# Kernel optimization log

Measured on AMD Instinct MI355X. Metric: run time of the kernel, lower is better.

The kernel has to match this reference:

```python
import jax, jax.numpy as jnp
import numpy as np

T = 1048576          # number of time steps in the trace
SIGMA_NUM = 8
EPSILON_NUM = 8
FEAT = 2 + SIGMA_NUM + EPSILON_NUM  # [t, r_obs, sigmas..., epsilons...]


def setup_inputs() -> dict:
    key = jax.random.key(0)
    ks = jax.random.split(key, 6)
    trace = jax.random.normal(ks[0], (T, FEAT), dtype=jnp.float32)
    # column 0 is time: sorted grid with small dt so the 1M-step recurrence stays bounded
    trace = trace.at[:, 0].set(jnp.arange(T, dtype=jnp.float32) * 1e-3)
    # column 1 row 0 is the initial rate; keep it positive-ish
    trace = trace.at[0, 1].set(0.05)
    sigma_W = jax.random.normal(ks[1], (1, SIGMA_NUM), dtype=jnp.float32) * 0.01
    sigma_b = jax.random.normal(ks[2], (1,), dtype=jnp.float32) * 0.01
    eps_W = jax.random.normal(ks[3], (1, EPSILON_NUM), dtype=jnp.float32) * 0.01
    k = jnp.abs(jax.random.normal(ks[4], (1,), dtype=jnp.float32)) * 0.1
    theta = jnp.abs(jax.random.normal(ks[5], (1,), dtype=jnp.float32)) * 0.05
    return {"trace_data": trace, "sigma_W": sigma_W, "sigma_b": sigma_b,
            "eps_W": eps_W, "k": k, "theta": theta}


def reference(trace_data, sigma_W, sigma_b, eps_W, k, theta):
    S, E = SIGMA_NUM, EPSILON_NUM
    t = trace_data[:, 0]
    dts = t[1:] - t[:-1]                                   # [T-1]
    # sigma/epsilon projections depend only on trace data -> vectorize outside scan
    sig = trace_data[:-1, 2:2 + S] @ sigma_W[0] + sigma_b[0]   # [T-1]
    eps = trace_data[:-1, 2 + S:2 + S + E] @ eps_W[0]          # [T-1]
    kk = k[0]
    th = theta[0]
    r0 = trace_data[0, 1]

    def step(r, x):
        dt, s, e = x
        ode = r + kk * (th - r) * dt
        sde = s * jnp.sqrt(jnp.abs(r * dt)) * e
        r_next = ode + sde
        return r_next, r_next

    _, r_predicts = jax.lax.scan(step, r0, (dts, sig, eps))   # [T-1]
    regs = 2.0 * kk * th - sig ** 2                           # [T-1]
    return r_predicts, regs, dts
```

## Files before the change

kernel.cpp:

```cpp
#include <hip/hip_runtime.h>
#include <math.h>

#define NSTEPS   1048575
#define FEAT     18
#define NB1      1024
#define NT1      256
#define NQ       (NB1 * NT1)
#define SLOTS    608
#define WBYTES   (SLOTS * 16)

#define GLDS16(g, l) \
    __builtin_amdgcn_global_load_lds((const __attribute__((address_space(1))) void*)(g), \
                                     (__attribute__((address_space(3))) void*)(l), 16, 0, 0)

#define WAIT_VM0()   asm volatile("s_waitcnt vmcnt(0)" ::: "memory")
#define WAIT_LGKM0() asm volatile("s_waitcnt lgkmcnt(0)" ::: "memory")

#define GSTEP(dd, cc) { \
    float a   = fmaf(-k, (dd), 1.f); \
    float b   = kth * (dd); \
    float ar  = fabsf(r); \
    float sq  = sqrtf(ar); \
    float inv = (ar > 1e-30f) ? rsqrtf(ar) : 0.f; \
    float g   = fmaf(0.5f * (cc), copysignf(inv, r), a); \
    r = fmaf((cc), sq, fmaf(a, r, b)); \
    P *= g; }

#define FSTEP(dd, cc) { \
    float a = fmaf(-k, (dd), 1.f); \
    float b = kth * (dd); \
    rr = fmaf((cc), sqrtf(fabsf(rr)), fmaf(a, rr, b)); }

#define DOTSE(S0,S1,S2,S3,S4,S5,S6,S7, E0,E1,E2,E3,E4,E5,E6,E7, sigv, epv) { \
    float sig_ = sb0; \
    sig_ = fmaf((S0), sw0, sig_); sig_ = fmaf((S1), sw1, sig_); \
    sig_ = fmaf((S2), sw2, sig_); sig_ = fmaf((S3), sw3, sig_); \
    sig_ = fmaf((S4), sw4, sig_); sig_ = fmaf((S5), sw5, sig_); \
    sig_ = fmaf((S6), sw6, sig_); sig_ = fmaf((S7), sw7, sig_); \
    float ep_ = 0.f; \
    ep_ = fmaf((E0), ew0, ep_); ep_ = fmaf((E1), ew1, ep_); \
    ep_ = fmaf((E2), ew2, ep_); ep_ = fmaf((E3), ew3, ep_); \
    ep_ = fmaf((E4), ew4, ep_); ep_ = fmaf((E5), ew5, ep_); \
    ep_ = fmaf((E6), ew6, ep_); ep_ = fmaf((E7), ew7, ep_); \
    (sigv) = sig_; (epv) = ep_; }

#define EXTRACT_COMPUTE(JROW) { \
    const float4* sr = (const float4*)lw + 19 * (JROW); \
    float4 u0 = sr[0],  u1  = sr[1],  u2  = sr[2],  u3  = sr[3],  u4  = sr[4]; \
    float4 u5 = sr[5],  u6  = sr[6],  u7  = sr[7],  u8  = sr[8]; \
    float4 u9 = sr[9],  u10 = sr[10], u11 = sr[11], u12 = sr[12], u13 = sr[13]; \
    float4 u14 = sr[14], u15 = sr[15], u16 = sr[16], u17 = sr[17]; \
    tfirst = u0.x; t3 = u13.z; \
    d0 = u4.z  - u0.x;  d1 = u9.x - u4.z;  d2 = u13.z - u9.x; \
    float ep0, ep1, ep2; \
    DOTSE(u0.z,u0.w,u1.x,u1.y,u1.z,u1.w,u2.x,u2.y, \
          u2.z,u2.w,u3.x,u3.y,u3.z,u3.w,u4.x,u4.y, sig0, ep0) \
    DOTSE(u5.x,u5.y,u5.z,u5.w,u6.x,u6.y,u6.z,u6.w, \
          u7.x,u7.y,u7.z,u7.w,u8.x,u8.y,u8.z,u8.w, sig1, ep1) \
    DOTSE(u9.z,u9.w,u10.x,u10.y,u10.z,u10.w,u11.x,u11.y, \
          u11.z,u11.w,u12.x,u12.y,u12.z,u12.w,u13.x,u13.y, sig2, ep2) \
    DOTSE(u14.x,u14.y,u14.z,u14.w,u15.x,u15.y,u15.z,u15.w, \
          u16.x,u16.y,u16.z,u16.w,u17.x,u17.y,u17.z,u17.w, sig3, ep3) \
    c0v = sig0 * ep0 * sqrtf(fabsf(d0)); \
    c1v = sig1 * ep1 * sqrtf(fabsf(d1)); \
    c2v = sig2 * ep2 * sqrtf(fabsf(d2)); }

__device__ __forceinline__ void stage_pass(const float4* __restrict__ base4,
                                           char* lds_wave, int lane)
{
    int jr = lane / 19;
    int ic = lane - 19 * jr;
#pragma unroll
    for (int i = 0; i < 10; ++i) {
        int col = (ic == 18) ? 17 : ic;
        const float4* src = base4 + (18 * jr + col);
        if (i < 9) {
            GLDS16(src, lds_wave + i * 1024);
        } else if (lane < 32) {
            GLDS16(src, lds_wave + 9 * 1024);
        }
        jr += 3; ic += 7;
        if (ic >= 19) { ic -= 19; ++jr; }
    }
}

__device__ __forceinline__ void wave_scan_affine(float& A, float& B, int lane) {
#pragma unroll
    for (int d = 1; d < 64; d <<= 1) {
        float pA = __shfl_up(A, d, 64);
        float pB = __shfl_up(B, d, 64);
        if (lane >= d) { B = fmaf(A, pB, B); A *= pA; }
    }
}

__global__ void __launch_bounds__(NT1) cir_prep(
    const float* __restrict__ trace,
    const float* __restrict__ sW, const float* __restrict__ sb,
    const float* __restrict__ eW, const float* __restrict__ kp,
    const float* __restrict__ thp,
    float* __restrict__ out,
    float2* __restrict__ dc, float2* __restrict__ pref, float2* __restrict__ agg)
{
    __shared__ __align__(16) char stage[4 * WBYTES];
    __shared__ float wAs[4], wBs[4];

    const int tid = threadIdx.x, lane = tid & 63, wid = tid >> 6, bid = blockIdx.x;
    const long c = (long)bid * NT1 + tid;
    char* lw = stage + wid * WBYTES;
    const float4* t4 = (const float4*)trace;
    const long waveQuad = (long)bid * NT1 + (long)wid * 64;

    stage_pass(t4 + waveQuad * 18, lw, lane);

    const float k = kp[0], th = thp[0], kth = k * th, tkth2 = 2.f * kth;
    const float sb0 = sb[0];
    const float sw0 = sW[0], sw1 = sW[1], sw2 = sW[2], sw3 = sW[3];
    const float sw4 = sW[4], sw5 = sW[5], sw6 = sW[6], sw7 = sW[7];
    const float ew0 = eW[0], ew1 = eW[1], ew2 = eW[2], ew3 = eW[3];
    const float ew4 = eW[4], ew5 = eW[5], ew6 = eW[6], ew7 = eW[7];
    const float t0g = trace[0], r0v = trace[1];

    float tfirst, t3, d0, d1, d2, c0v, c1v, c2v, sig0, sig1, sig2, sig3, ep3;

    WAIT_VM0();
    if (lane < 32) EXTRACT_COMPUTE(lane)
    WAIT_LGKM0();

    stage_pass(t4 + (waveQuad + 32) * 18, lw, lane);
    WAIT_VM0();
    if (lane >= 32) EXTRACT_COMPUTE(lane - 32)

    float tnext = __shfl_down(tfirst, 1, 64);
    if (lane == 63)
        tnext = (c + 1 < (long)NQ) ? trace[(c * 4 + 4) * FEAT] : 0.f;
    float d3 = tnext - t3;
    const long n0 = c * 4;
    float c3v = sig3 * ep3 * sqrtf(fabsf(d3));
    if (n0 + 4 > NSTEPS) { d3 = 0.f; c3v = 0.f; }

    out[NSTEPS + n0 + 0] = fmaf(-sig0, sig0, tkth2);
    out[NSTEPS + n0 + 1] = fmaf(-sig1, sig1, tkth2);
    out[NSTEPS + n0 + 2] = fmaf(-sig2, sig2, tkth2);
    out[2L * NSTEPS + n0 + 0] = d0;
    out[2L * NSTEPS + n0 + 1] = d1;
    out[2L * NSTEPS + n0 + 2] = d2;
    if (n0 + 4 <= NSTEPS) {
        out[NSTEPS + n0 + 3] = fmaf(-sig3, sig3, tkth2);
        out[2L * NSTEPS + n0 + 3] = d3;
    }

    float4* dc4 = (float4*)dc;
    dc4[2 * c]     = make_float4(d0, c0v, d1, c1v);
    dc4[2 * c + 1] = make_float4(d2, c2v, d3, c3v);

    float s = th + (r0v - th) * __expf(-k * (tfirst - t0g));
    float r = s, P = 1.f;
    GSTEP(d0, c0v)
    GSTEP(d1, c1v)
    GSTEP(d2, c2v)
    GSTEP(d3, c3v)
    float A = P, Bv = fmaf(-P, s, r);

    float iA = A, iB = Bv;
    wave_scan_affine(iA, iB, lane);
    if (lane == 63) { wAs[wid] = iA; wBs[wid] = iB; }
    __syncthreads();
    if (wid == 0) {
        float aA = (lane < 4) ? wAs[lane] : 1.f;
        float aB = (lane < 4) ? wBs[lane] : 0.f;
        wave_scan_affine(aA, aB, lane);
        if (lane < 4) { wAs[lane] = aA; wBs[lane] = aB; }
    }
    __syncthreads();
    float weA = 1.f, weB = 0.f;
    if (wid > 0) { weA = wAs[wid - 1]; weB = wBs[wid - 1]; }
    float eA = __shfl_up(iA, 1, 64), eB = __shfl_up(iB, 1, 64);
    if (lane == 0) { eA = 1.f; eB = 0.f; }

    pref[c] = make_float2(eA * weA, fmaf(eA, weB, eB));
    if (tid == 0) agg[bid] = make_float2(wAs[3], wBs[3]);
}

__global__ void __launch_bounds__(NT1) cir_final(
    const float* __restrict__ trace,
    const float* __restrict__ kp, const float* __restrict__ thp,
    const float2* __restrict__ dc, const float2* __restrict__ pref,
    const float2* __restrict__ agg,
    float* __restrict__ out)
{
    __shared__ float2 incs[NB1];
    __shared__ float wA2[4], wB2[4];

    const int tid = threadIdx.x, lane = tid & 63, wid = tid >> 6, bid = blockIdx.x;
    const long c = (long)bid * NT1 + tid;
    const float k = kp[0], th = thp[0], kth = k * th;
    const float r0v = trace[1];

    float2 a0 = agg[4 * tid + 0], a1 = agg[4 * tid + 1];
    float2 a2 = agg[4 * tid + 2], a3 = agg[4 * tid + 3];
    float cA = a0.x, cB = a0.y;
    cB = fmaf(a1.x, cB, a1.y); cA *= a1.x;
    cB = fmaf(a2.x, cB, a2.y); cA *= a2.x;
    cB = fmaf(a3.x, cB, a3.y); cA *= a3.x;

    float iA = cA, iB = cB;
    wave_scan_affine(iA, iB, lane);
    if (lane == 63) { wA2[wid] = iA; wB2[wid] = iB; }
    __syncthreads();
    if (wid == 0) {
        float aA = (lane < 4) ? wA2[lane] : 1.f;
        float aB = (lane < 4) ? wB2[lane] : 0.f;
        wave_scan_affine(aA, aB, lane);
        if (lane < 4) { wA2[lane] = aA; wB2[lane] = aB; }
    }
    __syncthreads();
    float weA = 1.f, weB = 0.f;
    if (wid > 0) { weA = wA2[wid - 1]; weB = wB2[wid - 1]; }
    float eA = __shfl_up(iA, 1, 64), eB = __shfl_up(iB, 1, 64);
    if (lane == 0) { eA = 1.f; eB = 0.f; }
    float EA = eA * weA, EB = fmaf(eA, weB, eB);

    float xA = a0.x * EA,  xB = fmaf(a0.x, EB, a0.y);
    incs[4 * tid + 0] = make_float2(xA, xB);
    xB = fmaf(a1.x, xB, a1.y); xA *= a1.x;
    incs[4 * tid + 1] = make_float2(xA, xB);
    xB = fmaf(a2.x, xB, a2.y); xA *= a2.x;
    incs[4 * tid + 2] = make_float2(xA, xB);
    xB = fmaf(a3.x, xB, a3.y); xA *= a3.x;
    incs[4 * tid + 3] = make_float2(xA, xB);
    __syncthreads();

    float beA = 1.f, beB = 0.f;
    if (bid > 0) { float2 p = incs[bid - 1]; beA = p.x; beB = p.y; }

    const float4* dc4 = (const float4*)dc;
    float4 q0 = dc4[2 * c], q1 = dc4[2 * c + 1];
    float2 pr = pref[c];
    float FA = pr.x * beA;
    float FB = fmaf(pr.x, beB, pr.y);
    float rr = fmaf(FA, r0v, FB);
    float4 ov;
    FSTEP(q0.x, q0.y) ov.x = rr;
    FSTEP(q0.z, q0.w) ov.y = rr;
    FSTEP(q1.x, q1.y) ov.z = rr;
    FSTEP(q1.z, q1.w) ov.w = rr;
    long nb = 4 * c;
    if (nb + 4 <= NSTEPS) {
        *(float4*)(out + nb) = ov;
    } else {
        out[nb + 0] = ov.x;
        out[nb + 1] = ov.y;
        out[nb + 2] = ov.z;
    }
}

extern "C" void kernel_launch(void* const* d_in, const int* in_sizes, int n_in,
                              void* d_out, int out_size, void* d_ws, size_t ws_size,
                              hipStream_t stream)
{
    const float* trace = (const float*)d_in[0];
    const float* sW    = (const float*)d_in[1];
    const float* sb    = (const float*)d_in[2];
    const float* eW    = (const float*)d_in[3];
    const float* kp    = (const float*)d_in[4];
    const float* thp   = (const float*)d_in[5];
    float* out = (float*)d_out;

    float2* dc   = (float2*)d_ws;
    float2* pref = dc + 4L * NQ;
    float2* agg  = pref + NQ;

    cir_prep<<<NB1, NT1, 0, stream>>>(trace, sW, sb, eW, kp, thp, out, dc, pref, agg);
    cir_final<<<NB1, NT1, 0, stream>>>(trace, kp, thp, dc, pref, agg, out);
}
```

Measured before the change: 124.2 us.

## Use single-wave prep blocks with 4096 aggregates and issue both LDS stages upfront

The prep kernel now runs one 64-thread wave per block, which removes the intra-block cross-wave scan and both __syncthreads barriers. It also issues both LDS staging passes before a single wait rather than serialising them. The final kernel scans 4096 per-wave aggregates (16 per thread) instead of 1024 and indexes the block prefix per wave. This trades barrier and serialisation cost in prep for a longer serial chain in the final kernel and twice the LDS per block.

```diff
diff --git a/kernel.cpp b/kernel.cpp
--- a/kernel.cpp
+++ b/kernel.cpp
@@ -3,9 +3,11 @@
 
 #define NSTEPS   1048575
 #define FEAT     18
-#define NB1      1024
-#define NT1      256
+#define NB1      4096
+#define NT1      64
 #define NQ       (NB1 * NT1)
+#define NB2      1024
+#define NT2      256
 #define SLOTS    608
 #define WBYTES   (SLOTS * 16)
 
@@ -14,7 +16,6 @@
                                      (__attribute__((address_space(3))) void*)(l), 16, 0, 0)
 
 #define WAIT_VM0()   asm volatile("s_waitcnt vmcnt(0)" ::: "memory")
-#define WAIT_LGKM0() asm volatile("s_waitcnt lgkmcnt(0)" ::: "memory")
 
 #define GSTEP(dd, cc) { \
     float a   = fmaf(-k, (dd), 1.f); \
@@ -66,7 +67,7 @@
     c2v = sig2 * ep2 * sqrtf(fabsf(d2)); }
 
 __device__ __forceinline__ void stage_pass(const float4* __restrict__ base4,
-                                           char* lds_wave, int lane)
+                                           char* lds_buf, int lane)
 {
     int jr = lane / 19;
     int ic = lane - 19 * jr;
@@ -75,9 +76,9 @@
         int col = (ic == 18) ? 17 : ic;
         const float4* src = base4 + (18 * jr + col);
         if (i < 9) {
-            GLDS16(src, lds_wave + i * 1024);
+            GLDS16(src, lds_buf + i * 1024);
         } else if (lane < 32) {
-            GLDS16(src, lds_wave + 9 * 1024);
+            GLDS16(src, lds_buf + 9 * 1024);
         }
         jr += 3; ic += 7;
         if (ic >= 19) { ic -= 19; ++jr; }
@@ -101,16 +102,16 @@
     float* __restrict__ out,
     float2* __restrict__ dc, float2* __restrict__ pref, float2* __restrict__ agg)
 {
-    __shared__ __align__(16) char stage[4 * WBYTES];
-    __shared__ float wAs[4], wBs[4];
-
-    const int tid = threadIdx.x, lane = tid & 63, wid = tid >> 6, bid = blockIdx.x;
-    const long c = (long)bid * NT1 + tid;
-    char* lw = stage + wid * WBYTES;
+    __shared__ __align__(16) char stage[2 * WBYTES];
+
+    const int lane = threadIdx.x;
+    const int bid = blockIdx.x;
+    const long c = (long)bid * NT1 + lane;
     const float4* t4 = (const float4*)trace;
-    const long waveQuad = (long)bid * NT1 + (long)wid * 64;
-
-    stage_pass(t4 + waveQuad * 18, lw, lane);
+    const long blockQuad = (long)bid * NT1;
+
+    stage_pass(t4 + blockQuad * 18,        stage,          lane);
+    stage_pass(t4 + (blockQuad + 32) * 18, stage + WBYTES, lane);
 
     const float k = kp[0], th = thp[0], kth = k * th, tkth2 = 2.f * kth;
     const float sb0 = sb[0];
@@ -123,12 +124,11 @@
     float tfirst, t3, d0, d1, d2, c0v, c1v, c2v, sig0, sig1, sig2, sig3, ep3;
 
     WAIT_VM0();
-    if (lane < 32) EXTRACT_COMPUTE(lane)
-    WAIT_LGKM0();
-
-    stage_pass(t4 + (waveQuad + 32) * 18, lw, lane);
-    WAIT_VM0();
-    if (lane >= 32) EXTRACT_COMPUTE(lane - 32)
+    {
+        char* lw = stage + ((lane < 32) ? 0 : WBYTES);
+        const int jrow = lane & 31;
+        EXTRACT_COMPUTE(jrow)
+    }
 
     float tnext = __shfl_down(tfirst, 1, 64);
     if (lane == 63)
@@ -163,25 +163,13 @@
 
     float iA = A, iB = Bv;
     wave_scan_affine(iA, iB, lane);
-    if (lane == 63) { wAs[wid] = iA; wBs[wid] = iB; }
-    __syncthreads();
-    if (wid == 0) {
-        float aA = (lane < 4) ? wAs[lane] : 1.f;
-        float aB = (lane < 4) ? wBs[lane] : 0.f;
-        wave_scan_affine(aA, aB, lane);
-        if (lane < 4) { wAs[lane] = aA; wBs[lane] = aB; }
-    }
-    __syncthreads();
-    float weA = 1.f, weB = 0.f;
-    if (wid > 0) { weA = wAs[wid - 1]; weB = wBs[wid - 1]; }
     float eA = __shfl_up(iA, 1, 64), eB = __shfl_up(iB, 1, 64);
     if (lane == 0) { eA = 1.f; eB = 0.f; }
-
-    pref[c] = make_float2(eA * weA, fmaf(eA, weB, eB));
-    if (tid == 0) agg[bid] = make_float2(wAs[3], wBs[3]);
-}
-
-__global__ void __launch_bounds__(NT1) cir_final(
+    pref[c] = make_float2(eA, eB);
+    if (lane == 63) agg[bid] = make_float2(iA, iB);
+}
+
+__global__ void __launch_bounds__(NT2) cir_final(
     const float* __restrict__ trace,
     const float* __restrict__ kp, const float* __restrict__ thp,
     const float2* __restrict__ dc, const float2* __restrict__ pref,
@@ -192,16 +180,16 @@
     __shared__ float wA2[4], wB2[4];
 
     const int tid = threadIdx.x, lane = tid & 63, wid = tid >> 6, bid = blockIdx.x;
-    const long c = (long)bid * NT1 + tid;
+    const long c = (long)bid * NT2 + tid;
     const float k = kp[0], th = thp[0], kth = k * th;
     const float r0v = trace[1];
 
-    float2 a0 = agg[4 * tid + 0], a1 = agg[4 * tid + 1];
-    float2 a2 = agg[4 * tid + 2], a3 = agg[4 * tid + 3];
-    float cA = a0.x, cB = a0.y;
-    cB = fmaf(a1.x, cB, a1.y); cA *= a1.x;
-    cB = fmaf(a2.x, cB, a2.y); cA *= a2.x;
-    cB = fmaf(a3.x, cB, a3.y); cA *= a3.x;
+    float2 av[16];
+#pragma unroll
+    for (int i = 0; i < 16; ++i) av[i] = agg[16 * tid + i];
+    float cA = av[0].x, cB = av[0].y;
+#pragma unroll
+    for (int i = 1; i < 16; ++i) { cB = fmaf(av[i].x, cB, av[i].y); cA *= av[i].x; }
 
     float iA = cA, iB = cB;
     wave_scan_affine(iA, iB, lane);
@@ -220,18 +208,17 @@
     if (lane == 0) { eA = 1.f; eB = 0.f; }
     float EA = eA * weA, EB = fmaf(eA, weB, eB);
 
-    float xA = a0.x * EA,  xB = fmaf(a0.x, EB, a0.y);
-    incs[4 * tid + 0] = make_float2(xA, xB);
-    xB = fmaf(a1.x, xB, a1.y); xA *= a1.x;
-    incs[4 * tid + 1] = make_float2(xA, xB);
-    xB = fmaf(a2.x, xB, a2.y); xA *= a2.x;
-    incs[4 * tid + 2] = make_float2(xA, xB);
-    xB = fmaf(a3.x, xB, a3.y); xA *= a3.x;
-    incs[4 * tid + 3] = make_float2(xA, xB);
+    float xA = EA, xB = EB;
+#pragma unroll
+    for (int i = 0; i < 16; ++i) {
+        xB = fmaf(av[i].x, xB, av[i].y); xA *= av[i].x;
+        incs[16 * tid + i] = make_float2(xA, xB);
+    }
     __syncthreads();
 
+    const int pblk = 4 * bid + wid;
     float beA = 1.f, beB = 0.f;
-    if (bid > 0) { float2 p = incs[bid - 1]; beA = p.x; beB = p.y; }
+    if (pblk > 0) { float2 p = incs[pblk - 1]; beA = p.x; beB = p.y; }
 
     const float4* dc4 = (const float4*)dc;
     float4 q0 = dc4[2 * c], q1 = dc4[2 * c + 1];
@@ -271,5 +258,5 @@
     float2* agg  = pref + NQ;
 
     cir_prep<<<NB1, NT1, 0, stream>>>(trace, sW, sb, eW, kp, thp, out, dc, pref, agg);
-    cir_final<<<NB1, NT1, 0, stream>>>(trace, kp, thp, dc, pref, agg, out);
-}
+    cir_final<<<NB2, NT2, 0, stream>>>(trace, kp, thp, dc, pref, agg, out);
+}
```

New measurement: 127.7 us. 2.8% more time.
